# Optimization experiments

Hardware: AMD Instinct MI355X
Metric: run time of the kernel (lower is better)

The kernel has to match this reference:

```python
import jax, jax.numpy as jnp
import numpy as np

ALPHA = 0.2  # LeakyReLU negative slope

def setup_inputs() -> dict:
    key = jax.random.key(0)
    k1, k2 = jax.random.split(key)
    K, N = 4096, 1024
    x = jax.random.normal(k1, (K, N), dtype=jnp.float32)
    # xavier_uniform with gain 1.414 on shape (2N, 1)
    limit = 1.414 * np.sqrt(6.0 / (2 * N + 1))
    w = jax.random.uniform(k2, (2 * N, 1), dtype=jnp.float32, minval=-limit, maxval=limit)
    return {"x": x, "w": w}

def reference(x, w):
    # Faithful to: e[i,j] = leakyrelu(concat(x[i], x[j]) @ w)
    # Split w into halves -> outer-sum score (same math, no KxK x 2N intermediate).
    N = x.shape[1]
    w1 = w[:N, 0]   # (N,)
    w2 = w[N:, 0]   # (N,)
    s1 = x @ w1     # (K,)
    s2 = x @ w2     # (K,)
    e = jax.nn.leaky_relu(s1[:, None] + s2[None, :], negative_slope=ALPHA)  # (K, K)
    attention = jax.nn.softmax(e, axis=1)  # dropout p=0.0 -> identity
    h = attention @ x  # (K, N)
    return h
```

## Files before the change

kernel.cpp:

```cpp
#include <hip/hip_runtime.h>

#define KDIM 4096
#define NDIM 1024
#define ALPHA 0.2f
#define LOG2E 1.4426950408889634f
#define CCH 256
#define RCH 16
#define PFL 256

__device__ __align__(16) float g_s1L[KDIM];
__device__ __align__(16) float g_s2L[KDIM];
__device__ __align__(16) float g_E [2 * KDIM];
__device__ __align__(16) float g_F1[KDIM];
__device__ __align__(16) float g_F2[KDIM];
__device__ __align__(16) float g_rZ[KDIM];
__device__ __align__(16) int   g_t  [KDIM];
__device__ __align__(16) int   g_sig[KDIM];
__device__ __align__(16) float g_cs [CCH][2 * NDIM];
__device__ __align__(16) float g_pre[CCH][2 * NDIM];
__device__ __align__(16) float g_tot[2 * NDIM];

__global__ __launch_bounds__(256) void k_dots(const float* __restrict__ x,
                                              const float* __restrict__ w){
  const int wid = threadIdx.x >> 6, lane = threadIdx.x & 63;
  const int row = blockIdx.x * 4 + wid;
  const float* xr = x + (size_t)row * NDIM;
  float d1 = 0.f, d2 = 0.f;
  #pragma unroll
  for (int q = 0; q < 4; ++q){
    const int off = q * 256 + lane * 4;
    float4 X  = *(const float4*)(xr + off);
    float4 W1 = *(const float4*)(w + off);
    float4 W2 = *(const float4*)(w + NDIM + off);
    d1 = fmaf(X.x, W1.x, fmaf(X.y, W1.y, fmaf(X.z, W1.z, fmaf(X.w, W1.w, d1))));
    d2 = fmaf(X.x, W2.x, fmaf(X.y, W2.y, fmaf(X.z, W2.z, fmaf(X.w, W2.w, d2))));
  }
  #pragma unroll
  for (int m = 32; m >= 1; m >>= 1){
    d1 += __shfl_xor(d1, m, 64);
    d2 += __shfl_xor(d2, m, 64);
  }
  if (lane == 0){
    g_s1L[row] = d1 * LOG2E;
    g_s2L[row] = d2 * LOG2E;
  }
}

__global__ __launch_bounds__(1024) void k_escan(){
  __shared__ float red[1024];
  const int tid = threadIdx.x;
  const float4 s2v = *(const float4*)&g_s2L[tid * 4];
  red[tid] = fmaxf(fmaxf(s2v.x, s2v.y), fmaxf(s2v.z, s2v.w));
  __syncthreads();
  #pragma unroll
  for (int s = 512; s >= 1; s >>= 1){
    if (tid < s) red[tid] = fmaxf(red[tid], red[tid + s]);
    __syncthreads();
  }
  const float m2 = red[0];

  float4 e0, e1;
  e0.x = __builtin_amdgcn_exp2f(s2v.x); e0.y = __builtin_amdgcn_exp2f(ALPHA * s2v.x);
  e0.z = __builtin_amdgcn_exp2f(s2v.y); e0.w = __builtin_amdgcn_exp2f(ALPHA * s2v.y);
  e1.x = __builtin_amdgcn_exp2f(s2v.z); e1.y = __builtin_amdgcn_exp2f(ALPHA * s2v.z);
  e1.z = __builtin_amdgcn_exp2f(s2v.w); e1.w = __builtin_amdgcn_exp2f(ALPHA * s2v.w);
  *(float4*)&g_E[tid * 8]     = e0;
  *(float4*)&g_E[tid * 8 + 4] = e1;

  const float4 s1v = *(const float4*)&g_s1L[tid * 4];
  float4 F1, F2;
  {
    float t, mL;
    t = s1v.x + m2; mL = fmaxf(t, ALPHA * t);
    F1.x = __builtin_amdgcn_exp2f(s1v.x - mL);
    F2.x = __builtin_amdgcn_exp2f(fmaf(ALPHA, s1v.x, -mL));
    t = s1v.y + m2; mL = fmaxf(t, ALPHA * t);
    F1.y = __builtin_amdgcn_exp2f(s1v.y - mL);
    F2.y = __builtin_amdgcn_exp2f(fmaf(ALPHA, s1v.y, -mL));
    t = s1v.z + m2; mL = fmaxf(t, ALPHA * t);
    F1.z = __builtin_amdgcn_exp2f(s1v.z - mL);
    F2.z = __builtin_amdgcn_exp2f(fmaf(ALPHA, s1v.z, -mL));
    t = s1v.w + m2; mL = fmaxf(t, ALPHA * t);
    F1.w = __builtin_amdgcn_exp2f(s1v.w - mL);
    F2.w = __builtin_amdgcn_exp2f(fmaf(ALPHA, s1v.w, -mL));
  }
  *(float4*)&g_F1[tid * 4] = F1;
  *(float4*)&g_F2[tid * 4] = F2;
}

__global__ __launch_bounds__(256) void k_rank(){
  __shared__ __align__(16) float s2s[KDIM];
  const int tid = threadIdx.x;
  #pragma unroll
  for (int q = 0; q < 4; ++q)
    ((float4*)s2s)[q * 256 + tid] = ((const float4*)g_s2L)[q * 256 + tid];
  __syncthreads();
  const int grp = tid >> 4, sub = tid & 15;
  const int o = blockIdx.x * 16 + grp;
  int cnt = 0;
  if (o < KDIM){
    const float val = s2s[o];
    #pragma unroll 4
    for (int m = 0; m < 64; ++m){
      const int q4 = sub * 64 + ((m + sub) & 63);
      const float4 v = ((const float4*)s2s)[q4];
      const int j0 = q4 * 4;
      cnt += (v.x > val || (v.x == val && (j0    ) < o));
      cnt += (v.y > val || (v.y == val && (j0 + 1) < o));
      cnt += (v.z > val || (v.z == val && (j0 + 2) < o));
      cnt += (v.w > val || (v.w == val && (j0 + 3) < o));
    }
  } else {
    const float thr = -g_s1L[o - KDIM];
    #pragma unroll 4
    for (int m = 0; m < 64; ++m){
      const int q4 = sub * 64 + ((m + sub) & 63);
      const float4 v = ((const float4*)s2s)[q4];
      cnt += (v.x >= thr) + (v.y >= thr) + (v.z >= thr) + (v.w >= thr);
    }
  }
  cnt += __shfl_xor(cnt, 1, 64); cnt += __shfl_xor(cnt, 2, 64);
  cnt += __shfl_xor(cnt, 4, 64); cnt += __shfl_xor(cnt, 8, 64);
  if (sub == 0){
    if (o < KDIM) g_sig[cnt] = o;
    else          g_t[o - KDIM] = cnt;
  }
}

__global__ __launch_bounds__(1024) void k_zscan(){
  __shared__ __align__(16) float z1L[KDIM + 1];
  __shared__ __align__(16) float z2L[KDIM + 1];
  __shared__ float wsum1[16], wsum2[16];
  const int tid = threadIdx.x, lane = tid & 63, wid = tid >> 6;
  float v1[4], v2[4];
  #pragma unroll
  for (int q = 0; q < 4; ++q){
    const int j = g_sig[tid * 4 + q];
    v1[q] = g_E[2 * j];
    v2[q] = g_E[2 * j + 1];
  }
  const float s1 = v1[0] + v1[1] + v1[2] + v1[3];
  const float s2 = v2[0] + v2[1] + v2[2] + v2[3];
  float i1 = s1, i2 = s2;
  #pragma unroll
  for (int d = 1; d < 64; d <<= 1){
    const float t1 = __shfl_up(i1, d, 64);
    const float t2 = __shfl_up(i2, d, 64);
    if (lane >= d){ i1 += t1; i2 += t2; }
  }
  if (lane == 63){ wsum1[wid] = i1; wsum2[wid] = i2; }
  __syncthreads();
  float w1 = 0.f, w2 = 0.f;
  for (int k = 0; k < wid; ++k){ w1 += wsum1[k]; w2 += wsum2[k]; }
  float e1 = w1 + i1 - s1;
  float e2 = w2 + i2 - s2;
  #pragma unroll
  for (int q = 0; q < 4; ++q){
    z1L[tid * 4 + q] = e1; e1 += v1[q];
    z2L[tid * 4 + q] = e2; e2 += v2[q];
  }
  if (tid == 1023){ z1L[KDIM] = e1; z2L[KDIM] = e2; }
  __syncthreads();
  const float z2T = z2L[KDIM];
  #pragma unroll
  for (int q = 0; q < 4; ++q){
    const int i = q * 1024 + tid;
    const int t = g_t[i];
    const float Z = fmaf(g_F1[i], z1L[t], g_F2[i] * (z2T - z2L[t]));
    g_rZ[i] = 1.0f / Z;
  }
}

__global__ __launch_bounds__(256) void k_chunksum(const float* __restrict__ x){
  __shared__ int   js [RCH];
  __shared__ float e1s[RCH], e2s[RCH];
  const int c = blockIdx.x, tid = threadIdx.x;
  if (tid < RCH){
    const int j = g_sig[c * RCH + tid];
    js[tid]  = j;
    e1s[tid] = g_E[2 * j];
    e2s[tid] = g_E[2 * j + 1];
  }
  __syncthreads();
  float4 a1 = {0.f, 0.f, 0.f, 0.f}, a2 = {0.f, 0.f, 0.f, 0.f};
  #pragma unroll
  for (int r = 0; r < RCH; ++r){
    const float4 xv = *(const float4*)(x + (size_t)js[r] * NDIM + tid * 4);
    const float e1 = e1s[r], e2 = e2s[r];
    a1.x = fmaf(e1, xv.x, a1.x); a1.y = fmaf(e1, xv.y, a1.y);
    a1.z = fmaf(e1, xv.z, a1.z); a1.w = fmaf(e1, xv.w, a1.w);
    a2.x = fmaf(e2, xv.x, a2.x); a2.y = fmaf(e2, xv.y, a2.y);
    a2.z = fmaf(e2, xv.z, a2.z); a2.w = fmaf(e2, xv.w, a2.w);
  }
  *(float4*)&g_cs[c][tid * 4]        = a1;
  *(float4*)&g_cs[c][NDIM + tid * 4] = a2;
}

__global__ __launch_bounds__(256) void k_chunkscan(){
  __shared__ float TL[CCH][32];
  __shared__ float SS[8][32];
  const int tid = threadIdx.x;
  const int s = tid >> 5, k = tid & 31;
  const int col = blockIdx.x * 32 + k;
  float run = 0.f;
  #pragma unroll 8
  for (int m = 0; m < 32; ++m){
    const float v = g_cs[s * 32 + m][col];
    TL[s * 32 + m][k] = v;
    run += v;
  }
  SS[s][k] = run;
  __syncthreads();
  if (s == 0){
    float acc = 0.f;
    #pragma unroll
    for (int t = 0; t < 8; ++t){
      const float v = SS[t][k];
      SS[t][k] = acc;
      acc += v;
    }
    g_tot[col] = acc;
  }
  __syncthreads();
  run = SS[s][k];
  #pragma unroll 8
  for (int m = 0; m < 32; ++m){
    g_pre[s * 32 + m][col] = run;
    run += TL[s * 32 + m][k];
  }
}

__global__ __launch_bounds__(256) void k_emit(const float* __restrict__ x,
                                              float* __restrict__ out){
  __shared__ int    js [RCH];
  __shared__ float  e1s[RCH], e2s[RCH];
  __shared__ int    cnt[RCH + 1];
  __shared__ int    off[RCH + 2];
  __shared__ int    pos[RCH + 1];
  __shared__ int    ilist[KDIM];
  __shared__ float4 pfl[PFL];
  const int c = blockIdx.x, tid = threadIdx.x;
  const bool last = (c == CCH - 1);
  const int nbuck = last ? RCH + 1 : RCH;
  if (tid < RCH){
    const int j = g_sig[c * RCH + tid];
    js[tid]  = j;
    e1s[tid] = g_E[2 * j];
    e2s[tid] = g_E[2 * j + 1];
  }
  if (tid <= RCH) cnt[tid] = 0;
  __syncthreads();

  const int tbase = c * RCH;
  int myi[16], myr[16];
  #pragma unroll
  for (int q = 0; q < 16; ++q){
    const int i = q * 256 + tid;
    const int t = g_t[i];
    const int r = t - tbase;
    const bool in = (r >= 0) && (r < nbuck);
    myi[q] = i;
    myr[q] = in ? r : -1;
    if (in) atomicAdd(&cnt[r], 1);
  }
  __syncthreads();
  if (tid == 0){
    int run = 0;
    #pragma unroll
    for (int r = 0; r <= RCH; ++r){
      const int v = cnt[r];
      off[r] = run; pos[r] = run;
      run += v;
    }
    off[RCH + 1] = run;
  }
  __syncthreads();
  #pragma unroll
  for (int q = 0; q < 16; ++q){
    if (myr[q] >= 0){
      const int p = atomicAdd(&pos[myr[q]], 1);
      ilist[p] = myi[q];
      if (p < PFL)
        pfl[p] = make_float4(g_F1[myi[q]], g_F2[myi[q]], g_rZ[myi[q]], 0.f);
    }
  }
  __syncthreads();

  float4 a1 = *(const float4*)&g_pre[c][tid * 4];
  float4 a2 = *(const float4*)&g_pre[c][NDIM + tid * 4];
  const float4 t2 = *(const float4*)&g_tot[NDIM + tid * 4];
  float4 v[RCH];
  #pragma unroll
  for (int r = 0; r < RCH; ++r)
    v[r] = *(const float4*)(x + (size_t)js[r] * NDIM + tid * 4);

  #pragma unroll
  for (int r = 0; r < RCH; ++r){
    for (int e = off[r]; e < off[r + 1]; ++e){
      const int i = ilist[e];
      float F1, F2, rz;
      if (e < PFL){ const float4 pf = pfl[e]; F1 = pf.x; F2 = pf.y; rz = pf.z; }
      else        { F1 = g_F1[i]; F2 = g_F2[i]; rz = g_rZ[i]; }
      float4 h;
      h.x = fmaf(F1, a1.x, F2 * (t2.x - a2.x)) * rz;
      h.y = fmaf(F1, a1.y, F2 * (t2.y - a2.y)) * rz;
      h.z = fmaf(F1, a1.z, F2 * (t2.z - a2.z)) * rz;
      h.w = fmaf(F1, a1.w, F2 * (t2.w - a2.w)) * rz;
      *(float4*)(out + (size_t)i * NDIM + tid * 4) = h;
    }
    const float e1 = e1s[r], e2 = e2s[r];
    const float4 xv = v[r];
    a1.x = fmaf(e1, xv.x, a1.x); a1.y = fmaf(e1, xv.y, a1.y);
    a1.z = fmaf(e1, xv.z, a1.z); a1.w = fmaf(e1, xv.w, a1.w);
    a2.x = fmaf(e2, xv.x, a2.x); a2.y = fmaf(e2, xv.y, a2.y);
    a2.z = fmaf(e2, xv.z, a2.z); a2.w = fmaf(e2, xv.w, a2.w);
  }
  if (last){
    for (int e = off[RCH]; e < off[RCH + 1]; ++e){
      const int i = ilist[e];
      float F1, F2, rz;
      if (e < PFL){ const float4 pf = pfl[e]; F1 = pf.x; F2 = pf.y; rz = pf.z; }
      else        { F1 = g_F1[i]; F2 = g_F2[i]; rz = g_rZ[i]; }
      float4 h;
      h.x = fmaf(F1, a1.x, F2 * (t2.x - a2.x)) * rz;
      h.y = fmaf(F1, a1.y, F2 * (t2.y - a2.y)) * rz;
      h.z = fmaf(F1, a1.z, F2 * (t2.z - a2.z)) * rz;
      h.w = fmaf(F1, a1.w, F2 * (t2.w - a2.w)) * rz;
      *(float4*)(out + (size_t)i * NDIM + tid * 4) = h;
    }
  }
}

extern "C" void kernel_launch(void* const* d_in, const int* in_sizes, int n_in,
                              void* d_out, int out_size, void* d_ws, size_t ws_size,
                              hipStream_t stream){
  const float* x = (const float*)d_in[0];
  const float* w = (const float*)d_in[1];
  float* out = (float*)d_out;
  (void)in_sizes; (void)n_in; (void)out_size; (void)d_ws; (void)ws_size;

  k_dots     <<<dim3(1024), dim3(256),  0, stream>>>(x, w);
  k_escan    <<<dim3(1),    dim3(1024), 0, stream>>>();
  k_rank     <<<dim3(512),  dim3(256),  0, stream>>>();
  k_zscan    <<<dim3(1),    dim3(1024), 0, stream>>>();
  k_chunksum <<<dim3(CCH),  dim3(256),  0, stream>>>(x);
  k_chunkscan<<<dim3(64),   dim3(256),  0, stream>>>();
  k_emit     <<<dim3(CCH),  dim3(256),  0, stream>>>(x, out);
}
```

Measured before the change: 118.6 us.

## Fold exp precompute into dots and normaliser scan into chunk pipeline

Computes the exponential factors directly in the dot-product kernel, dropping the max-shift, and removes the single-block escan kernel. The single-block zscan kernel is replaced by per-chunk weight sums, a small scan in chunkscan, and reciprocal normalisers computed on the fly in emit. The rank kernel's shared-memory access pattern becomes strided by sub-lane. This removes two serial single-block launches at the cost of losing the max-subtraction stabilisation, which risks overflow for larger score ranges.

```diff
diff --git a/kernel.cpp b/kernel.cpp
--- a/kernel.cpp
+++ b/kernel.cpp
@@ -13,12 +13,14 @@
 __device__ __align__(16) float g_E [2 * KDIM];
 __device__ __align__(16) float g_F1[KDIM];
 __device__ __align__(16) float g_F2[KDIM];
-__device__ __align__(16) float g_rZ[KDIM];
 __device__ __align__(16) int   g_t  [KDIM];
 __device__ __align__(16) int   g_sig[KDIM];
 __device__ __align__(16) float g_cs [CCH][2 * NDIM];
 __device__ __align__(16) float g_pre[CCH][2 * NDIM];
 __device__ __align__(16) float g_tot[2 * NDIM];
+__device__ __align__(16) float g_cz [2 * CCH];
+__device__ __align__(16) float g_zpre[2 * CCH];
+__device__ __align__(16) float g_ztot[2];
 
 __global__ __launch_bounds__(256) void k_dots(const float* __restrict__ x,
                                               const float* __restrict__ w){
@@ -41,51 +43,14 @@
     d2 += __shfl_xor(d2, m, 64);
   }
   if (lane == 0){
-    g_s1L[row] = d1 * LOG2E;
-    g_s2L[row] = d2 * LOG2E;
-  }
-}
-
-__global__ __launch_bounds__(1024) void k_escan(){
-  __shared__ float red[1024];
-  const int tid = threadIdx.x;
-  const float4 s2v = *(const float4*)&g_s2L[tid * 4];
-  red[tid] = fmaxf(fmaxf(s2v.x, s2v.y), fmaxf(s2v.z, s2v.w));
-  __syncthreads();
-  #pragma unroll
-  for (int s = 512; s >= 1; s >>= 1){
-    if (tid < s) red[tid] = fmaxf(red[tid], red[tid + s]);
-    __syncthreads();
-  }
-  const float m2 = red[0];
-
-  float4 e0, e1;
-  e0.x = __builtin_amdgcn_exp2f(s2v.x); e0.y = __builtin_amdgcn_exp2f(ALPHA * s2v.x);
-  e0.z = __builtin_amdgcn_exp2f(s2v.y); e0.w = __builtin_amdgcn_exp2f(ALPHA * s2v.y);
-  e1.x = __builtin_amdgcn_exp2f(s2v.z); e1.y = __builtin_amdgcn_exp2f(ALPHA * s2v.z);
-  e1.z = __builtin_amdgcn_exp2f(s2v.w); e1.w = __builtin_amdgcn_exp2f(ALPHA * s2v.w);
-  *(float4*)&g_E[tid * 8]     = e0;
-  *(float4*)&g_E[tid * 8 + 4] = e1;
-
-  const float4 s1v = *(const float4*)&g_s1L[tid * 4];
-  float4 F1, F2;
-  {
-    float t, mL;
-    t = s1v.x + m2; mL = fmaxf(t, ALPHA * t);
-    F1.x = __builtin_amdgcn_exp2f(s1v.x - mL);
-    F2.x = __builtin_amdgcn_exp2f(fmaf(ALPHA, s1v.x, -mL));
-    t = s1v.y + m2; mL = fmaxf(t, ALPHA * t);
-    F1.y = __builtin_amdgcn_exp2f(s1v.y - mL);
-    F2.y = __builtin_amdgcn_exp2f(fmaf(ALPHA, s1v.y, -mL));
-    t = s1v.z + m2; mL = fmaxf(t, ALPHA * t);
-    F1.z = __builtin_amdgcn_exp2f(s1v.z - mL);
-    F2.z = __builtin_amdgcn_exp2f(fmaf(ALPHA, s1v.z, -mL));
-    t = s1v.w + m2; mL = fmaxf(t, ALPHA * t);
-    F1.w = __builtin_amdgcn_exp2f(s1v.w - mL);
-    F2.w = __builtin_amdgcn_exp2f(fmaf(ALPHA, s1v.w, -mL));
-  }
-  *(float4*)&g_F1[tid * 4] = F1;
-  *(float4*)&g_F2[tid * 4] = F2;
+    const float s1 = d1 * LOG2E, s2 = d2 * LOG2E;
+    g_s1L[row] = s1;
+    g_s2L[row] = s2;
+    g_E[2 * row]     = __builtin_amdgcn_exp2f(s2);
+    g_E[2 * row + 1] = __builtin_amdgcn_exp2f(ALPHA * s2);
+    g_F1[row] = __builtin_amdgcn_exp2f(s1);
+    g_F2[row] = __builtin_amdgcn_exp2f(ALPHA * s1);
+  }
 }
 
 __global__ __launch_bounds__(256) void k_rank(){
@@ -102,7 +67,7 @@
     const float val = s2s[o];
     #pragma unroll 4
     for (int m = 0; m < 64; ++m){
-      const int q4 = sub * 64 + ((m + sub) & 63);
+      const int q4 = m * 16 + sub;
       const float4 v = ((const float4*)s2s)[q4];
       const int j0 = q4 * 4;
       cnt += (v.x > val || (v.x == val && (j0    ) < o));
@@ -114,7 +79,7 @@
     const float thr = -g_s1L[o - KDIM];
     #pragma unroll 4
     for (int m = 0; m < 64; ++m){
-      const int q4 = sub * 64 + ((m + sub) & 63);
+      const int q4 = m * 16 + sub;
       const float4 v = ((const float4*)s2s)[q4];
       cnt += (v.x >= thr) + (v.y >= thr) + (v.z >= thr) + (v.w >= thr);
     }
@@ -124,50 +89,6 @@
   if (sub == 0){
     if (o < KDIM) g_sig[cnt] = o;
     else          g_t[o - KDIM] = cnt;
-  }
-}
-
-__global__ __launch_bounds__(1024) void k_zscan(){
-  __shared__ __align__(16) float z1L[KDIM + 1];
-  __shared__ __align__(16) float z2L[KDIM + 1];
-  __shared__ float wsum1[16], wsum2[16];
-  const int tid = threadIdx.x, lane = tid & 63, wid = tid >> 6;
-  float v1[4], v2[4];
-  #pragma unroll
-  for (int q = 0; q < 4; ++q){
-    const int j = g_sig[tid * 4 + q];
-    v1[q] = g_E[2 * j];
-    v2[q] = g_E[2 * j + 1];
-  }
-  const float s1 = v1[0] + v1[1] + v1[2] + v1[3];
-  const float s2 = v2[0] + v2[1] + v2[2] + v2[3];
-  float i1 = s1, i2 = s2;
-  #pragma unroll
-  for (int d = 1; d < 64; d <<= 1){
-    const float t1 = __shfl_up(i1, d, 64);
-    const float t2 = __shfl_up(i2, d, 64);
-    if (lane >= d){ i1 += t1; i2 += t2; }
-  }
-  if (lane == 63){ wsum1[wid] = i1; wsum2[wid] = i2; }
-  __syncthreads();
-  float w1 = 0.f, w2 = 0.f;
-  for (int k = 0; k < wid; ++k){ w1 += wsum1[k]; w2 += wsum2[k]; }
-  float e1 = w1 + i1 - s1;
-  float e2 = w2 + i2 - s2;
-  #pragma unroll
-  for (int q = 0; q < 4; ++q){
-    z1L[tid * 4 + q] = e1; e1 += v1[q];
-    z2L[tid * 4 + q] = e2; e2 += v2[q];
-  }
-  if (tid == 1023){ z1L[KDIM] = e1; z2L[KDIM] = e2; }
-  __syncthreads();
-  const float z2T = z2L[KDIM];
-  #pragma unroll
-  for (int q = 0; q < 4; ++q){
-    const int i = q * 1024 + tid;
-    const int t = g_t[i];
-    const float Z = fmaf(g_F1[i], z1L[t], g_F2[i] * (z2T - z2L[t]));
-    g_rZ[i] = 1.0f / Z;
   }
 }
 
@@ -182,6 +103,12 @@
     e2s[tid] = g_E[2 * j + 1];
   }
   __syncthreads();
+  if (tid == 0){
+    float a = 0.f, b = 0.f;
+    #pragma unroll
+    for (int r = 0; r < RCH; ++r){ a += e1s[r]; b += e2s[r]; }
+    g_cz[2 * c] = a; g_cz[2 * c + 1] = b;
+  }
   float4 a1 = {0.f, 0.f, 0.f, 0.f}, a2 = {0.f, 0.f, 0.f, 0.f};
   #pragma unroll
   for (int r = 0; r < RCH; ++r){
@@ -228,6 +155,31 @@
     g_pre[s * 32 + m][col] = run;
     run += TL[s * 32 + m][k];
   }
+  if (blockIdx.x == 0 && tid < 64){
+    float v1[4], v2[4];
+    #pragma unroll
+    for (int q = 0; q < 4; ++q){
+      v1[q] = g_cz[2 * (tid * 4 + q)];
+      v2[q] = g_cz[2 * (tid * 4 + q) + 1];
+    }
+    const float s1 = v1[0] + v1[1] + v1[2] + v1[3];
+    const float s2 = v2[0] + v2[1] + v2[2] + v2[3];
+    float i1 = s1, i2 = s2;
+    #pragma unroll
+    for (int d = 1; d < 64; d <<= 1){
+      const float t1 = __shfl_up(i1, d, 64);
+      const float t2 = __shfl_up(i2, d, 64);
+      if (tid >= d){ i1 += t1; i2 += t2; }
+    }
+    float e1 = i1 - s1, e2 = i2 - s2;
+    #pragma unroll
+    for (int q = 0; q < 4; ++q){
+      g_zpre[2 * (tid * 4 + q)]     = e1;
+      g_zpre[2 * (tid * 4 + q) + 1] = e2;
+      e1 += v1[q]; e2 += v2[q];
+    }
+    if (tid == 63){ g_ztot[0] = e1; g_ztot[1] = e2; }
+  }
 }
 
 __global__ __launch_bounds__(256) void k_emit(const float* __restrict__ x,
@@ -238,7 +190,7 @@
   __shared__ int    off[RCH + 2];
   __shared__ int    pos[RCH + 1];
   __shared__ int    ilist[KDIM];
-  __shared__ float4 pfl[PFL];
+  __shared__ float2 pfl[PFL];
   const int c = blockIdx.x, tid = threadIdx.x;
   const bool last = (c == CCH - 1);
   const int nbuck = last ? RCH + 1 : RCH;
@@ -281,7 +233,7 @@
       const int p = atomicAdd(&pos[myr[q]], 1);
       ilist[p] = myi[q];
       if (p < PFL)
-        pfl[p] = make_float4(g_F1[myi[q]], g_F2[myi[q]], g_rZ[myi[q]], 0.f);
+        pfl[p] = make_float2(g_F1[myi[q]], g_F2[myi[q]]);
     }
   }
   __syncthreads();
@@ -289,6 +241,8 @@
   float4 a1 = *(const float4*)&g_pre[c][tid * 4];
   float4 a2 = *(const float4*)&g_pre[c][NDIM + tid * 4];
   const float4 t2 = *(const float4*)&g_tot[NDIM + tid * 4];
+  float za1 = g_zpre[2 * c], za2 = g_zpre[2 * c + 1];
+  const float zt2 = g_ztot[1];
   float4 v[RCH];
   #pragma unroll
   for (int r = 0; r < RCH; ++r)
@@ -298,9 +252,10 @@
   for (int r = 0; r < RCH; ++r){
     for (int e = off[r]; e < off[r + 1]; ++e){
       const int i = ilist[e];
-      float F1, F2, rz;
-      if (e < PFL){ const float4 pf = pfl[e]; F1 = pf.x; F2 = pf.y; rz = pf.z; }
-      else        { F1 = g_F1[i]; F2 = g_F2[i]; rz = g_rZ[i]; }
+      float F1, F2;
+      if (e < PFL){ const float2 pf = pfl[e]; F1 = pf.x; F2 = pf.y; }
+      else        { F1 = g_F1[i]; F2 = g_F2[i]; }
+      const float rz = 1.0f / fmaf(F1, za1, F2 * (zt2 - za2));
       float4 h;
       h.x = fmaf(F1, a1.x, F2 * (t2.x - a2.x)) * rz;
       h.y = fmaf(F1, a1.y, F2 * (t2.y - a2.y)) * rz;
@@ -309,6 +264,7 @@
       *(float4*)(out + (size_t)i * NDIM + tid * 4) = h;
     }
     const float e1 = e1s[r], e2 = e2s[r];
+    za1 += e1; za2 += e2;
     const float4 xv = v[r];
     a1.x = fmaf(e1, xv.x, a1.x); a1.y = fmaf(e1, xv.y, a1.y);
     a1.z = fmaf(e1, xv.z, a1.z); a1.w = fmaf(e1, xv.w, a1.w);
@@ -318,9 +274,10 @@
   if (last){
     for (int e = off[RCH]; e < off[RCH + 1]; ++e){
       const int i = ilist[e];
-      float F1, F2, rz;
-      if (e < PFL){ const float4 pf = pfl[e]; F1 = pf.x; F2 = pf.y; rz = pf.z; }
-      else        { F1 = g_F1[i]; F2 = g_F2[i]; rz = g_rZ[i]; }
+      float F1, F2;
+      if (e < PFL){ const float2 pf = pfl[e]; F1 = pf.x; F2 = pf.y; }
+      else        { F1 = g_F1[i]; F2 = g_F2[i]; }
+      const float rz = 1.0f / fmaf(F1, za1, F2 * (zt2 - za2));
       float4 h;
       h.x = fmaf(F1, a1.x, F2 * (t2.x - a2.x)) * rz;
       h.y = fmaf(F1, a1.y, F2 * (t2.y - a2.y)) * rz;
@@ -339,11 +296,9 @@
   float* out = (float*)d_out;
   (void)in_sizes; (void)n_in; (void)out_size; (void)d_ws; (void)ws_size;
 
-  k_dots     <<<dim3(1024), dim3(256),  0, stream>>>(x, w);
-  k_escan    <<<dim3(1),    dim3(1024), 0, stream>>>();
-  k_rank     <<<dim3(512),  dim3(256),  0, stream>>>();
-  k_zscan    <<<dim3(1),    dim3(1024), 0, stream>>>();
-  k_chunksum <<<dim3(CCH),  dim3(256),  0, stream>>>(x);
-  k_chunkscan<<<dim3(64),   dim3(256),  0, stream>>>();
-  k_emit     <<<dim3(CCH),  dim3(256),  0, stream>>>(x, out);
-}
+  k_dots     <<<dim3(1024), dim3(256), 0, stream>>>(x, w);
+  k_rank     <<<dim3(512),  dim3(256), 0, stream>>>();
+  k_chunksum <<<dim3(CCH),  dim3(256), 0, stream>>>(x);
+  k_chunkscan<<<dim3(64),   dim3(256), 0, stream>>>();
+  k_emit     <<<dim3(CCH),  dim3(256), 0, stream>>>(x, out);
+}
```

Result: faster. 102.6 us (-13.5%).
